# Performance work log

Measured on AMD Instinct MI355X. Metric: run time of the kernel, lower is better.

The kernel has to match this reference:

```python
import jax, jax.numpy as jnp
import numpy as np

C_OUT = 16
C_IN = 16
L0 = 64        # layer_sizes[0]
H = 128        # hidden width
D_IN = C_IN * L0  # 1024, flattened per-point input dim


def _uniform(key, shape, fan_in):
    bound = 1.0 / np.sqrt(fan_in)
    return jax.random.uniform(key, shape, jnp.float32, -bound, bound)


def setup_inputs() -> dict:
    key = jax.random.key(0)
    ks = jax.random.split(key, 7)
    x = jax.random.normal(ks[0], (65536, C_IN, L0), jnp.float32)
    # Stacked per-output-channel MLP weights (torch Linear transposed: [in, out])
    W1 = _uniform(ks[1], (C_OUT, D_IN, H), D_IN)
    b1 = _uniform(ks[2], (C_OUT, H), D_IN)
    W2 = _uniform(ks[3], (C_OUT, H, H), H)
    b2 = _uniform(ks[4], (C_OUT, H, H)[:2], H)
    W3 = _uniform(ks[5], (C_OUT, H, 1), H)
    b3 = _uniform(ks[6], (C_OUT, 1), H)
    return {"x": x, "W1": W1, "b1": b1, "W2": W2, "b2": b2, "W3": W3, "b3": b3}


def reference(x, W1, b1, W2, b2, W3, b3):
    # x: [N, C_in, L0] -> flatten per point to [N, D_IN]
    N = x.shape[0]
    xf = x.reshape(N, -1)
    # Batched per-output-channel GEMMs (replaces Python loop over channels_out)
    h = jax.nn.relu(jnp.einsum('nd,cdh->cnh', xf, W1) + b1[:, None, :])   # [C, N, H]
    h = jax.nn.relu(jnp.einsum('cnh,chk->cnk', h, W2) + b2[:, None, :])   # [C, N, H]
    out = jnp.einsum('cnh,cho->cno', h, W3) + b3[:, None, :]              # [C, N, 1]
    # squeeze(-1) then permute channel axis to the end: [N, C_out]
    return out[..., 0].T
```

## Files before the change

kernel.cpp:

```cpp
#include <hip/hip_runtime.h>
#include <cstdint>

typedef unsigned short u16;
typedef __attribute__((ext_vector_type(4))) float f32x4;
typedef __attribute__((ext_vector_type(8))) __bf16 bf16x8;
typedef __attribute__((ext_vector_type(8))) u16 u16x8;
typedef __attribute__((ext_vector_type(4))) u16 u16x4;

#define C_OUT 16
#define D_IN 1024
#define HDIM 128
#define NPTS 65536
#define BN 128
#define BK 64

__device__ __forceinline__ u16 f2bf(float f){
  uint32_t u = __builtin_bit_cast(uint32_t, f);
  u += 0x7FFFu + ((u >> 16) & 1u);
  return (u16)(u >> 16);
}

__device__ __forceinline__ void gload_lds16(const void* g, void* l){
  __builtin_amdgcn_global_load_lds((const __attribute__((address_space(1))) void*)g,
                                   (__attribute__((address_space(3))) void*)l, 16, 0, 0);
}

__global__ __launch_bounds__(256) void transpose_cvt(const float* __restrict__ src,
                                                     u16* __restrict__ dst, int R, int C){
  __shared__ float tile[32][33];
  int ch = blockIdx.z;
  int r0 = blockIdx.y * 32, c0 = blockIdx.x * 32;
  const float* s = src + (size_t)ch * R * C;
  u16* d = dst + (size_t)ch * R * C;
  int tx = threadIdx.x, ty = threadIdx.y;
  for (int i = ty; i < 32; i += 8) tile[i][tx] = s[(size_t)(r0 + i) * C + c0 + tx];
  __syncthreads();
  for (int i = ty; i < 32; i += 8) d[(size_t)(c0 + i) * R + r0 + tx] = f2bf(tile[tx][i]);
}

__global__ __launch_bounds__(256) void cvt_x_kernel(const float4* __restrict__ src,
                                                    u16x4* __restrict__ dst, int n4){
  int stride = gridDim.x * 256;
  for (int i = blockIdx.x * 256 + threadIdx.x; i < n4; i += stride){
    float4 v = src[i];
    u16x4 o = { f2bf(v.x), f2bf(v.y), f2bf(v.z), f2bf(v.w) };
    dst[i] = o;
  }
}

template<bool XBF16>
__global__ __launch_bounds__(256, 3) void mlp_fused(const void* __restrict__ xsrc,
    const u16* __restrict__ W1T, const u16* __restrict__ W2T,
    const float* __restrict__ b1, const float* __restrict__ b2,
    const float* __restrict__ W3, const float* __restrict__ b3,
    float* __restrict__ out){
  __shared__ __align__(16) u16 smem[2 * BN * BK];
  __shared__ float outb[BN];
  u16* As = smem;
  u16* Bs = smem + BN * BK;

  const int t = threadIdx.x;
  const int wave = t >> 6, lane = t & 63;
  const int q = lane >> 4, s = lane & 15;
  const int wr = (wave >> 1) * 64, wc = (wave & 1) * 64;
  const int c = blockIdx.x & 15;
  const int n0 = (blockIdx.x >> 4) * BN;

  const u16* w1c = W1T + (size_t)c * HDIM * D_IN;

  f32x4 acc[4][4];
#pragma unroll
  for (int i = 0; i < 4; i++)
#pragma unroll
    for (int j = 0; j < 4; j++) acc[i][j] = (f32x4){0.f, 0.f, 0.f, 0.f};

  for (int kt = 0; kt < D_IN / BK; kt++){
#pragma unroll
    for (int ii = 0; ii < 4; ii++){
      int hbase = wave * 32 + ii * 8;
      int h = hbase + (lane >> 3);
      int k = kt * BK + (((lane & 7) ^ (h & 7)) * 8);
      gload_lds16(w1c + (size_t)h * D_IN + k, &Bs[hbase * BK]);
    }
    if (XBF16){
      const u16* xb = (const u16*)xsrc;
#pragma unroll
      for (int ii = 0; ii < 4; ii++){
        int rbase = wave * 32 + ii * 8;
        int row = rbase + (lane >> 3);
        int k = kt * BK + (((lane & 7) ^ (row & 7)) * 8);
        gload_lds16(xb + (size_t)(n0 + row) * D_IN + k, &As[rbase * BK]);
      }
    } else {
      const float* xf = (const float*)xsrc;
#pragma unroll
      for (int rr = 0; rr < 4; rr++){
        int row = rr * 32 + (t >> 3);
        const float* srcp = xf + (size_t)(n0 + row) * D_IN + kt * BK + (t & 7) * 8;
        float4 v0 = *(const float4*)srcp;
        float4 v1 = *(const float4*)(srcp + 4);
        u16x8 p = { f2bf(v0.x), f2bf(v0.y), f2bf(v0.z), f2bf(v0.w),
                    f2bf(v1.x), f2bf(v1.y), f2bf(v1.z), f2bf(v1.w) };
        int sc = (t & 7) ^ (row & 7);
        *(u16x8*)&As[row * BK + sc * 8] = p;
      }
    }
    __syncthreads();
#pragma unroll
    for (int ks = 0; ks < 2; ks++){
      bf16x8 a[4], b[4];
#pragma unroll
      for (int i = 0; i < 4; i++){
        int m = wr + i * 16 + s;
        int ch = ks * 4 + q;
        a[i] = __builtin_bit_cast(bf16x8, *(const u16x8*)&As[m * BK + ((ch ^ (m & 7)) * 8)]);
      }
#pragma unroll
      for (int j = 0; j < 4; j++){
        int hh = wc + j * 16 + s;
        int ch = ks * 4 + q;
        b[j] = __builtin_bit_cast(bf16x8, *(const u16x8*)&Bs[hh * BK + ((ch ^ (hh & 7)) * 8)]);
      }
#pragma unroll
      for (int i = 0; i < 4; i++)
#pragma unroll
        for (int j = 0; j < 4; j++)
          acc[i][j] = __builtin_amdgcn_mfma_f32_16x16x32_bf16(a[i], b[j], acc[i][j], 0, 0, 0);
    }
    __syncthreads();
  }

  float b1v[4];
#pragma unroll
  for (int j = 0; j < 4; j++) b1v[j] = b1[c * HDIM + wc + j * 16 + s];
  u16* h1s = smem;
#pragma unroll
  for (int i = 0; i < 4; i++)
#pragma unroll
    for (int j = 0; j < 4; j++)
#pragma unroll
      for (int r = 0; r < 4; r++){
        float v = fmaxf(acc[i][j][r] + b1v[j], 0.f);
        int m = wr + i * 16 + q * 4 + r;
        int h = wc + j * 16 + s;
        h1s[m * HDIM + (((h >> 3) ^ (m & 7)) * 8) + (h & 7)] = f2bf(v);
      }
  __syncthreads();

  const u16* w2c = W2T + (size_t)c * HDIM * HDIM;
  f32x4 acc2[4][4];
#pragma unroll
  for (int i = 0; i < 4; i++)
#pragma unroll
    for (int j = 0; j < 4; j++) acc2[i][j] = (f32x4){0.f, 0.f, 0.f, 0.f};
#pragma unroll
  for (int ks = 0; ks < 4; ks++){
    bf16x8 a[4], b[4];
#pragma unroll
    for (int i = 0; i < 4; i++){
      int m = wr + i * 16 + s;
      int ch = ks * 4 + q;
      a[i] = __builtin_bit_cast(bf16x8, *(const u16x8*)&h1s[m * HDIM + ((ch ^ (m & 7)) * 8)]);
    }
#pragma unroll
    for (int j = 0; j < 4; j++){
      int col = wc + j * 16 + s;
      b[j] = __builtin_bit_cast(bf16x8, *(const u16x8*)(w2c + (size_t)col * HDIM + ks * 32 + q * 8));
    }
#pragma unroll
    for (int i = 0; i < 4; i++)
#pragma unroll
      for (int j = 0; j < 4; j++)
        acc2[i][j] = __builtin_amdgcn_mfma_f32_16x16x32_bf16(a[i], b[j], acc2[i][j], 0, 0, 0);
  }

  float b2v[4], w3v[4];
#pragma unroll
  for (int j = 0; j < 4; j++){
    b2v[j] = b2[c * HDIM + wc + j * 16 + s];
    w3v[j] = W3[c * HDIM + wc + j * 16 + s];
  }
  float part[4][4];
#pragma unroll
  for (int i = 0; i < 4; i++)
#pragma unroll
    for (int r = 0; r < 4; r++) part[i][r] = 0.f;
#pragma unroll
  for (int i = 0; i < 4; i++)
#pragma unroll
    for (int j = 0; j < 4; j++)
#pragma unroll
      for (int r = 0; r < 4; r++){
        float hv = fmaxf(acc2[i][j][r] + b2v[j], 0.f);
        part[i][r] = fmaf(hv, w3v[j], part[i][r]);
      }
#pragma unroll
  for (int mask = 1; mask <= 8; mask <<= 1)
#pragma unroll
    for (int i = 0; i < 4; i++)
#pragma unroll
      for (int r = 0; r < 4; r++) part[i][r] += __shfl_xor(part[i][r], mask, 64);

  if (s == 0 && wc == 0){
#pragma unroll
    for (int i = 0; i < 4; i++)
#pragma unroll
      for (int r = 0; r < 4; r++) outb[wr + i * 16 + q * 4 + r] = part[i][r];
  }
  __syncthreads();
  if (s == 0 && wc == 64){
#pragma unroll
    for (int i = 0; i < 4; i++)
#pragma unroll
      for (int r = 0; r < 4; r++) outb[wr + i * 16 + q * 4 + r] += part[i][r];
  }
  __syncthreads();
  if (t < BN) out[(size_t)(n0 + t) * C_OUT + c] = outb[t] + b3[c];
}

__global__ __launch_bounds__(256) void mlp_naive(const float* __restrict__ x,
    const float* __restrict__ W1, const float* __restrict__ b1,
    const float* __restrict__ W2, const float* __restrict__ b2,
    const float* __restrict__ W3, const float* __restrict__ b3,
    float* __restrict__ out){
  __shared__ float xs[16 * D_IN];
  __shared__ float h1[16 * HDIM];
  __shared__ float h2[16 * HDIM];
  int c = blockIdx.x & 15;
  int n0 = (blockIdx.x >> 4) * 16;
  int t = threadIdx.x;
  for (int i = t; i < 16 * D_IN; i += 256) xs[i] = x[(size_t)n0 * D_IN + i];
  __syncthreads();
  int h = t & 127, ng = t >> 7;
  const float* w1c = W1 + (size_t)c * D_IN * HDIM;
  float a1[8];
#pragma unroll
  for (int nn = 0; nn < 8; nn++) a1[nn] = 0.f;
  for (int d = 0; d < D_IN; d++){
    float w = w1c[(size_t)d * HDIM + h];
#pragma unroll
    for (int nn = 0; nn < 8; nn++) a1[nn] = fmaf(xs[(ng * 8 + nn) * D_IN + d], w, a1[nn]);
  }
  float bb = b1[c * HDIM + h];
#pragma unroll
  for (int nn = 0; nn < 8; nn++) h1[(ng * 8 + nn) * HDIM + h] = fmaxf(a1[nn] + bb, 0.f);
  __syncthreads();
  const float* w2c = W2 + (size_t)c * HDIM * HDIM;
  float a2[8];
#pragma unroll
  for (int nn = 0; nn < 8; nn++) a2[nn] = 0.f;
  for (int k = 0; k < HDIM; k++){
    float w = w2c[(size_t)k * HDIM + h];
#pragma unroll
    for (int nn = 0; nn < 8; nn++) a2[nn] = fmaf(h1[(ng * 8 + nn) * HDIM + k], w, a2[nn]);
  }
  bb = b2[c * HDIM + h];
#pragma unroll
  for (int nn = 0; nn < 8; nn++) h2[(ng * 8 + nn) * HDIM + h] = fmaxf(a2[nn] + bb, 0.f);
  __syncthreads();
  if (t < 16){
    float ssum = 0.f;
    for (int hh = 0; hh < HDIM; hh++) ssum = fmaf(h2[t * HDIM + hh], W3[c * HDIM + hh], ssum);
    out[(size_t)(n0 + t) * C_OUT + c] = ssum + b3[c];
  }
}

extern "C" void kernel_launch(void* const* d_in, const int* in_sizes, int n_in,
                              void* d_out, int out_size, void* d_ws, size_t ws_size,
                              hipStream_t stream){
  const float* x  = (const float*)d_in[0];
  const float* W1 = (const float*)d_in[1];
  const float* b1 = (const float*)d_in[2];
  const float* W2 = (const float*)d_in[3];
  const float* b2 = (const float*)d_in[4];
  const float* W3 = (const float*)d_in[5];
  const float* b3 = (const float*)d_in[6];
  float* out = (float*)d_out;

  const size_t W1T_elems = (size_t)C_OUT * HDIM * D_IN;
  const size_t W2T_elems = (size_t)C_OUT * HDIM * HDIM;
  const size_t ws_w_bytes = (W1T_elems + W2T_elems) * 2;
  const size_t xb_bytes   = (size_t)NPTS * D_IN * 2;

  if (ws_size < ws_w_bytes){
    mlp_naive<<<(NPTS / 16) * C_OUT, 256, 0, stream>>>(x, W1, b1, W2, b2, W3, b3, out);
    return;
  }

  u16* W1T = (u16*)d_ws;
  u16* W2T = W1T + W1T_elems;
  transpose_cvt<<<dim3(HDIM / 32, D_IN / 32, C_OUT), dim3(32, 8), 0, stream>>>(W1, W1T, D_IN, HDIM);
  transpose_cvt<<<dim3(HDIM / 32, HDIM / 32, C_OUT), dim3(32, 8), 0, stream>>>(W2, W2T, HDIM, HDIM);

  const int grid = (NPTS / BN) * C_OUT;
  if (ws_size >= ws_w_bytes + xb_bytes){
    u16* xb = W2T + W2T_elems;
    cvt_x_kernel<<<8192, 256, 0, stream>>>((const float4*)x, (u16x4*)xb, NPTS * D_IN / 4);
    mlp_fused<true><<<grid, 256, 0, stream>>>(xb, W1T, W2T, b1, b2, W3, b3, out);
  } else {
    mlp_fused<false><<<grid, 256, 0, stream>>>(x, W1T, W2T, b1, b2, W3, b3, out);
  }
}
```

Measured before the change: 714.3 us.

## Double-buffer GEMM1 tiles and convert fp32 x in-kernel, dropping pre-conversion pass

Removes the separate x-to-bf16 conversion kernel and instead loads fp32 x tiles into registers, prefetching the next tile while MFMAs run on the current one. LDS is doubled to hold two A/B stages, and the W1 tile for the next step is staged asynchronously. This avoids writing and rereading a full bf16 copy of x and overlaps loads with compute, at the cost of lower occupancy (launch bound 2) and twice the bytes per x tile read across channels.

```diff
diff --git a/kernel.cpp b/kernel.cpp
--- a/kernel.cpp
+++ b/kernel.cpp
@@ -5,7 +5,6 @@
 typedef __attribute__((ext_vector_type(4))) float f32x4;
 typedef __attribute__((ext_vector_type(8))) __bf16 bf16x8;
 typedef __attribute__((ext_vector_type(8))) u16 u16x8;
-typedef __attribute__((ext_vector_type(4))) u16 u16x4;
 
 #define C_OUT 16
 #define D_IN 1024
@@ -13,6 +12,7 @@
 #define NPTS 65536
 #define BN 128
 #define BK 64
+#define NKT (D_IN / BK)
 
 __device__ __forceinline__ u16 f2bf(float f){
   uint32_t u = __builtin_bit_cast(uint32_t, f);
@@ -38,26 +38,13 @@
   for (int i = ty; i < 32; i += 8) d[(size_t)(c0 + i) * R + r0 + tx] = f2bf(tile[tx][i]);
 }
 
-__global__ __launch_bounds__(256) void cvt_x_kernel(const float4* __restrict__ src,
-                                                    u16x4* __restrict__ dst, int n4){
-  int stride = gridDim.x * 256;
-  for (int i = blockIdx.x * 256 + threadIdx.x; i < n4; i += stride){
-    float4 v = src[i];
-    u16x4 o = { f2bf(v.x), f2bf(v.y), f2bf(v.z), f2bf(v.w) };
-    dst[i] = o;
-  }
-}
-
-template<bool XBF16>
-__global__ __launch_bounds__(256, 3) void mlp_fused(const void* __restrict__ xsrc,
+__global__ __launch_bounds__(256, 2) void mlp_fused(const float* __restrict__ x,
     const u16* __restrict__ W1T, const u16* __restrict__ W2T,
     const float* __restrict__ b1, const float* __restrict__ b2,
     const float* __restrict__ W3, const float* __restrict__ b3,
     float* __restrict__ out){
-  __shared__ __align__(16) u16 smem[2 * BN * BK];
+  __shared__ __align__(16) u16 smem[4 * BN * BK];
   __shared__ float outb[BN];
-  u16* As = smem;
-  u16* Bs = smem + BN * BK;
 
   const int t = threadIdx.x;
   const int wave = t >> 6, lane = t & 63;
@@ -67,6 +54,10 @@
   const int n0 = (blockIdx.x >> 4) * BN;
 
   const u16* w1c = W1T + (size_t)c * HDIM * D_IN;
+  const float* xblk = x + (size_t)n0 * D_IN;
+
+  const int arow = t >> 3;
+  const int acol = t & 7;
 
   f32x4 acc[4][4];
 #pragma unroll
@@ -74,38 +65,52 @@
 #pragma unroll
     for (int j = 0; j < 4; j++) acc[i][j] = (f32x4){0.f, 0.f, 0.f, 0.f};
 
-  for (int kt = 0; kt < D_IN / BK; kt++){
+  float4 va[4][2];
+
+  auto loadA = [&](int kt){
+#pragma unroll
+    for (int rr = 0; rr < 4; rr++){
+      const float* p = xblk + (size_t)(rr * 32 + arow) * D_IN + kt * BK + acol * 8;
+      va[rr][0] = *(const float4*)p;
+      va[rr][1] = *(const float4*)(p + 4);
+    }
+  };
+  auto stageB = [&](u16* Bs, int kt){
 #pragma unroll
     for (int ii = 0; ii < 4; ii++){
       int hbase = wave * 32 + ii * 8;
       int h = hbase + (lane >> 3);
       int k = kt * BK + (((lane & 7) ^ (h & 7)) * 8);
-      gload_lds16(w1c + (size_t)h * D_IN + k, &Bs[hbase * BK]);
-    }
-    if (XBF16){
-      const u16* xb = (const u16*)xsrc;
-#pragma unroll
-      for (int ii = 0; ii < 4; ii++){
-        int rbase = wave * 32 + ii * 8;
-        int row = rbase + (lane >> 3);
-        int k = kt * BK + (((lane & 7) ^ (row & 7)) * 8);
-        gload_lds16(xb + (size_t)(n0 + row) * D_IN + k, &As[rbase * BK]);
-      }
-    } else {
-      const float* xf = (const float*)xsrc;
-#pragma unroll
-      for (int rr = 0; rr < 4; rr++){
-        int row = rr * 32 + (t >> 3);
-        const float* srcp = xf + (size_t)(n0 + row) * D_IN + kt * BK + (t & 7) * 8;
-        float4 v0 = *(const float4*)srcp;
-        float4 v1 = *(const float4*)(srcp + 4);
-        u16x8 p = { f2bf(v0.x), f2bf(v0.y), f2bf(v0.z), f2bf(v0.w),
-                    f2bf(v1.x), f2bf(v1.y), f2bf(v1.z), f2bf(v1.w) };
-        int sc = (t & 7) ^ (row & 7);
-        *(u16x8*)&As[row * BK + sc * 8] = p;
-      }
-    }
-    __syncthreads();
+      gload_lds16(w1c + (size_t)h * D_IN + k, Bs + hbase * BK);
+    }
+  };
+  auto writeA = [&](u16* As){
+#pragma unroll
+    for (int rr = 0; rr < 4; rr++){
+      int row = rr * 32 + arow;
+      bf16x8 pv;
+      pv[0] = (__bf16)va[rr][0].x; pv[1] = (__bf16)va[rr][0].y;
+      pv[2] = (__bf16)va[rr][0].z; pv[3] = (__bf16)va[rr][0].w;
+      pv[4] = (__bf16)va[rr][1].x; pv[5] = (__bf16)va[rr][1].y;
+      pv[6] = (__bf16)va[rr][1].z; pv[7] = (__bf16)va[rr][1].w;
+      *(u16x8*)&As[row * BK + ((acol ^ (row & 7)) * 8)] = __builtin_bit_cast(u16x8, pv);
+    }
+  };
+
+  loadA(0);
+  stageB(smem + BN * BK, 0);
+  writeA(smem);
+  __syncthreads();
+
+  for (int kt = 0; kt < NKT; kt++){
+    u16* As  = smem + (kt & 1) * (2 * BN * BK);
+    u16* Bs  = As + BN * BK;
+    u16* Asn = smem + ((kt + 1) & 1) * (2 * BN * BK);
+    u16* Bsn = Asn + BN * BK;
+    if (kt < NKT - 1){
+      loadA(kt + 1);
+      stageB(Bsn, kt + 1);
+    }
 #pragma unroll
     for (int ks = 0; ks < 2; ks++){
       bf16x8 a[4], b[4];
@@ -127,6 +132,7 @@
         for (int j = 0; j < 4; j++)
           acc[i][j] = __builtin_amdgcn_mfma_f32_16x16x32_bf16(a[i], b[j], acc[i][j], 0, 0, 0);
     }
+    if (kt < NKT - 1) writeA(Asn);
     __syncthreads();
   }
 
@@ -280,7 +286,6 @@
   const size_t W1T_elems = (size_t)C_OUT * HDIM * D_IN;
   const size_t W2T_elems = (size_t)C_OUT * HDIM * HDIM;
   const size_t ws_w_bytes = (W1T_elems + W2T_elems) * 2;
-  const size_t xb_bytes   = (size_t)NPTS * D_IN * 2;
 
   if (ws_size < ws_w_bytes){
     mlp_naive<<<(NPTS / 16) * C_OUT, 256, 0, stream>>>(x, W1, b1, W2, b2, W3, b3, out);
@@ -293,11 +298,5 @@
   transpose_cvt<<<dim3(HDIM / 32, HDIM / 32, C_OUT), dim3(32, 8), 0, stream>>>(W2, W2T, HDIM, HDIM);
 
   const int grid = (NPTS / BN) * C_OUT;
-  if (ws_size >= ws_w_bytes + xb_bytes){
-    u16* xb = W2T + W2T_elems;
-    cvt_x_kernel<<<8192, 256, 0, stream>>>((const float4*)x, (u16x4*)xb, NPTS * D_IN / 4);
-    mlp_fused<true><<<grid, 256, 0, stream>>>(xb, W1T, W2T, b1, b2, W3, b3, out);
-  } else {
-    mlp_fused<false><<<grid, 256, 0, stream>>>(x, W1T, W2T, b1, b2, W3, b3, out);
-  }
-}
+  mlp_fused<<<grid, 256, 0, stream>>>(x, W1T, W2T, b1, b2, W3, b3, out);
+}
```

Result: slower. 974.5 us (+36.4%).

## Triple-buffer async LDS loads and enlarge block tile to 256 rows

Applied to the files above, without the earlier changes.

Replaces the single-buffered, fully synchronised K loop with a three-stage ring of LDS buffers. Direct global-to-LDS loads for tile kt+2 are issued while MFMAs consume tile kt, with explicit vmcnt waits and raw barriers in place of __syncthreads. The block tile doubles to 256 points with 512 threads, which halves W1 reloads per point, and the fp32-input fallback is removed. The much larger LDS footprint (about 147 KB) likely limits residency to one block per CU and cuts the number of resident waves.

```diff
diff --git a/kernel.cpp b/kernel.cpp
--- a/kernel.cpp
+++ b/kernel.cpp
@@ -11,8 +11,12 @@
 #define D_IN 1024
 #define HDIM 128
 #define NPTS 65536
-#define BN 128
+#define BM 256
 #define BK 64
+#define NKT (D_IN / BK)
+#define A_ELEMS (BM * BK)
+#define B_ELEMS (HDIM * BK)
+#define BUF_ELEMS (A_ELEMS + B_ELEMS)
 
 __device__ __forceinline__ u16 f2bf(float f){
   uint32_t u = __builtin_bit_cast(uint32_t, f);
@@ -48,64 +52,61 @@
   }
 }
 
-template<bool XBF16>
-__global__ __launch_bounds__(256, 3) void mlp_fused(const void* __restrict__ xsrc,
+__global__ __launch_bounds__(512, 2) void mlp_fused(const u16* __restrict__ xb,
     const u16* __restrict__ W1T, const u16* __restrict__ W2T,
     const float* __restrict__ b1, const float* __restrict__ b2,
     const float* __restrict__ W3, const float* __restrict__ b3,
     float* __restrict__ out){
-  __shared__ __align__(16) u16 smem[2 * BN * BK];
-  __shared__ float outb[BN];
-  u16* As = smem;
-  u16* Bs = smem + BN * BK;
+  __shared__ __align__(16) u16 smem[3 * BUF_ELEMS];
+  __shared__ float outb[BM];
 
   const int t = threadIdx.x;
   const int wave = t >> 6, lane = t & 63;
   const int q = lane >> 4, s = lane & 15;
-  const int wr = (wave >> 1) * 64, wc = (wave & 1) * 64;
+  const int wm = wave >> 1, wn = wave & 1;
+  const int wr = wm * 64, wc = wn * 64;
   const int c = blockIdx.x & 15;
-  const int n0 = (blockIdx.x >> 4) * BN;
+  const int n0 = (blockIdx.x >> 4) * BM;
 
   const u16* w1c = W1T + (size_t)c * HDIM * D_IN;
 
-  f32x4 acc[4][4];
-#pragma unroll
-  for (int i = 0; i < 4; i++)
-#pragma unroll
-    for (int j = 0; j < 4; j++) acc[i][j] = (f32x4){0.f, 0.f, 0.f, 0.f};
-
-  for (int kt = 0; kt < D_IN / BK; kt++){
+  auto stage = [&](int buf, int kt){
+    u16* As = smem + buf * BUF_ELEMS;
+    u16* Bs = As + A_ELEMS;
 #pragma unroll
     for (int ii = 0; ii < 4; ii++){
-      int hbase = wave * 32 + ii * 8;
+      int rbase = wave * 32 + ii * 8;
+      int row = rbase + (lane >> 3);
+      int k = kt * BK + (((lane & 7) ^ (row & 7)) * 8);
+      gload_lds16(xb + (size_t)(n0 + row) * D_IN + k, As + rbase * BK);
+    }
+#pragma unroll
+    for (int ii = 0; ii < 2; ii++){
+      int hbase = wave * 16 + ii * 8;
       int h = hbase + (lane >> 3);
       int k = kt * BK + (((lane & 7) ^ (h & 7)) * 8);
-      gload_lds16(w1c + (size_t)h * D_IN + k, &Bs[hbase * BK]);
-    }
-    if (XBF16){
-      const u16* xb = (const u16*)xsrc;
-#pragma unroll
-      for (int ii = 0; ii < 4; ii++){
-        int rbase = wave * 32 + ii * 8;
-        int row = rbase + (lane >> 3);
-        int k = kt * BK + (((lane & 7) ^ (row & 7)) * 8);
-        gload_lds16(xb + (size_t)(n0 + row) * D_IN + k, &As[rbase * BK]);
-      }
-    } else {
-      const float* xf = (const float*)xsrc;
-#pragma unroll
-      for (int rr = 0; rr < 4; rr++){
-        int row = rr * 32 + (t >> 3);
-        const float* srcp = xf + (size_t)(n0 + row) * D_IN + kt * BK + (t & 7) * 8;
-        float4 v0 = *(const float4*)srcp;
-        float4 v1 = *(const float4*)(srcp + 4);
-        u16x8 p = { f2bf(v0.x), f2bf(v0.y), f2bf(v0.z), f2bf(v0.w),
-                    f2bf(v1.x), f2bf(v1.y), f2bf(v1.z), f2bf(v1.w) };
-        int sc = (t & 7) ^ (row & 7);
-        *(u16x8*)&As[row * BK + sc * 8] = p;
-      }
-    }
-    __syncthreads();
+      gload_lds16(w1c + (size_t)h * D_IN + k, Bs + hbase * BK);
+    }
+  };
+
+  f32x4 acc[4][4];
+#pragma unroll
+  for (int i = 0; i < 4; i++)
+#pragma unroll
+    for (int j = 0; j < 4; j++) acc[i][j] = (f32x4){0.f, 0.f, 0.f, 0.f};
+
+  stage(0, 0);
+  stage(1, 1);
+  asm volatile("s_waitcnt vmcnt(6)" ::: "memory");
+  __builtin_amdgcn_s_barrier();
+  asm volatile("" ::: "memory");
+
+  int cur = 0;
+  for (int kt = 0; kt < NKT; kt++){
+    int nx2 = cur + 2; if (nx2 >= 3) nx2 -= 3;
+    if (kt + 2 < NKT) stage(nx2, kt + 2);
+    const u16* As = smem + cur * BUF_ELEMS;
+    const u16* Bs = As + A_ELEMS;
 #pragma unroll
     for (int ks = 0; ks < 2; ks++){
       bf16x8 a[4], b[4];
@@ -127,7 +128,11 @@
         for (int j = 0; j < 4; j++)
           acc[i][j] = __builtin_amdgcn_mfma_f32_16x16x32_bf16(a[i], b[j], acc[i][j], 0, 0, 0);
     }
-    __syncthreads();
+    if (kt + 2 < NKT) asm volatile("s_waitcnt vmcnt(6) lgkmcnt(0)" ::: "memory");
+    else              asm volatile("s_waitcnt vmcnt(0) lgkmcnt(0)" ::: "memory");
+    __builtin_amdgcn_s_barrier();
+    asm volatile("" ::: "memory");
+    cur++; if (cur == 3) cur = 0;
   }
 
   float b1v[4];
@@ -201,21 +206,21 @@
 #pragma unroll
       for (int r = 0; r < 4; r++) part[i][r] += __shfl_xor(part[i][r], mask, 64);
 
-  if (s == 0 && wc == 0){
+  if (s == 0 && wn == 0){
 #pragma unroll
     for (int i = 0; i < 4; i++)
 #pragma unroll
       for (int r = 0; r < 4; r++) outb[wr + i * 16 + q * 4 + r] = part[i][r];
   }
   __syncthreads();
-  if (s == 0 && wc == 64){
+  if (s == 0 && wn == 1){
 #pragma unroll
     for (int i = 0; i < 4; i++)
 #pragma unroll
       for (int r = 0; r < 4; r++) outb[wr + i * 16 + q * 4 + r] += part[i][r];
   }
   __syncthreads();
-  if (t < BN) out[(size_t)(n0 + t) * C_OUT + c] = outb[t] + b3[c];
+  if (t < BM) out[(size_t)(n0 + t) * C_OUT + c] = outb[t] + b3[c];
 }
 
 __global__ __launch_bounds__(256) void mlp_naive(const float* __restrict__ x,
@@ -282,22 +287,18 @@
   const size_t ws_w_bytes = (W1T_elems + W2T_elems) * 2;
   const size_t xb_bytes   = (size_t)NPTS * D_IN * 2;
 
-  if (ws_size < ws_w_bytes){
+  if (ws_size < ws_w_bytes + xb_bytes){
     mlp_naive<<<(NPTS / 16) * C_OUT, 256, 0, stream>>>(x, W1, b1, W2, b2, W3, b3, out);
     return;
   }
 
   u16* W1T = (u16*)d_ws;
   u16* W2T = W1T + W1T_elems;
+  u16* xb  = W2T + W2T_elems;
   transpose_cvt<<<dim3(HDIM / 32, D_IN / 32, C_OUT), dim3(32, 8), 0, stream>>>(W1, W1T, D_IN, HDIM);
   transpose_cvt<<<dim3(HDIM / 32, HDIM / 32, C_OUT), dim3(32, 8), 0, stream>>>(W2, W2T, HDIM, HDIM);
-
-  const int grid = (NPTS / BN) * C_OUT;
-  if (ws_size >= ws_w_bytes + xb_bytes){
-    u16* xb = W2T + W2T_elems;
-    cvt_x_kernel<<<8192, 256, 0, stream>>>((const float4*)x, (u16x4*)xb, NPTS * D_IN / 4);
-    mlp_fused<true><<<grid, 256, 0, stream>>>(xb, W1T, W2T, b1, b2, W3, b3, out);
-  } else {
-    mlp_fused<false><<<grid, 256, 0, stream>>>(x, W1T, W2T, b1, b2, W3, b3, out);
-  }
-}
+  cvt_x_kernel<<<8192, 256, 0, stream>>>((const float4*)x, (u16x4*)xb, NPTS * D_IN / 4);
+
+  const int grid = (NPTS / BM) * C_OUT;
+  mlp_fused<<<grid, 512, 0, stream>>>(xb, W1T, W2T, b1, b2, W3, b3, out);
+}
```

Result: slower. 870.4 us (+21.9%).
